# Kernel optimization log

Measured on AMD Instinct MI355X. Metric: run time of the kernel, lower is better.

Reference implementation:

```python
import jax, jax.numpy as jnp
import numpy as np

HEADS = 8
DIM_HEAD = 64
RMS_EPS = 1.1920929e-07  # torch default eps = finfo(fp32).eps


def rotate_half(x):
    x1, x2 = jnp.split(x, 2, axis=-1)
    return jnp.concatenate((-x2, x1), axis=-1)


def setup_inputs() -> dict:
    key = jax.random.key(0)
    k1, k2, k3, k4, k5 = jax.random.split(key, 5)
    b, n, dim = 2, 4096, 1024
    dim_hidden = HEADS * DIM_HEAD  # 512
    x = jax.random.normal(k1, (b, n, dim), dtype=jnp.float32)
    rotary_emb = jax.random.normal(k2, (n, DIM_HEAD), dtype=jnp.float32)
    rms_weight = jnp.ones((dim,), dtype=jnp.float32)
    w_qkv = jax.random.normal(k3, (dim, dim_hidden * 3), dtype=jnp.float32) * (dim ** -0.5)
    w_out = jax.random.normal(k4, (dim_hidden, dim), dtype=jnp.float32) * (dim_hidden ** -0.5)
    return {"x": x, "rotary_emb": rotary_emb, "rms_weight": rms_weight,
            "w_qkv": w_qkv, "w_out": w_out}


def reference(x, rotary_emb, rms_weight, w_qkv, w_out):
    b, n, dim = x.shape
    h, d = HEADS, DIM_HEAD
    # RMSNorm
    xn = x * jax.lax.rsqrt(jnp.mean(x * x, axis=-1, keepdims=True) + RMS_EPS) * rms_weight
    # QKV projection, rearrange 'b n (qkv h d) -> qkv b h n d'
    qkv = (xn @ w_qkv).reshape(b, n, 3, h, d).transpose(2, 0, 3, 1, 4)
    q, k, v = qkv[0], qkv[1], qkv[2]
    # RoPE
    cos, sin = jnp.cos(rotary_emb), jnp.sin(rotary_emb)  # (n, d) broadcasts over b,h
    q = q * cos + rotate_half(q) * sin
    k = k * cos + rotate_half(k) * sin
    q = q * (d ** -0.5)
    sim = jnp.einsum('bhid,bhjd->bhij', q, k)
    causal_mask = jnp.triu(jnp.ones((n, n), dtype=bool), 1)
    sim = jnp.where(causal_mask, -jnp.finfo(sim.dtype).max, sim)
    attn = jax.nn.softmax(sim, axis=-1)
    out = jnp.einsum('bhij,bhjd->bhid', attn, v)
    out = out.transpose(0, 2, 1, 3).reshape(b, n, h * d)  # 'b h n d -> b n (h d)'
    return out @ w_out
```

## Files before the change

kernel.cpp:

```cpp
#include <hip/hip_runtime.h>
#include <hip/hip_bf16.h>
#include <cstdint>

using bf16x8 = __attribute__((ext_vector_type(8))) __bf16;
using f32x4  = __attribute__((ext_vector_type(4))) float;

#define LOG2E 1.4426950408889634f

__device__ inline void gload16(__bf16* lds, const __bf16* g) {
    __builtin_amdgcn_global_load_lds((const __attribute__((address_space(1))) void*)g,
                                     (__attribute__((address_space(3))) void*)lds, 16, 0, 0);
}

__global__ __launch_bounds__(256) void rmsnorm_kernel(const float* __restrict__ x,
                                                      const float* __restrict__ w,
                                                      __bf16* __restrict__ xn) {
    const int row = blockIdx.x;
    const float4 v = reinterpret_cast<const float4*>(x + (size_t)row * 1024)[threadIdx.x];
    float ss = v.x * v.x + v.y * v.y + v.z * v.z + v.w * v.w;
#pragma unroll
    for (int i = 1; i < 64; i <<= 1) ss += __shfl_xor(ss, i);
    __shared__ float part[4];
    if ((threadIdx.x & 63) == 0) part[threadIdx.x >> 6] = ss;
    __syncthreads();
    const float total = part[0] + part[1] + part[2] + part[3];
    const float scale = rsqrtf(total * (1.0f / 1024.0f) + 1.1920929e-07f);
    const float4 wv = reinterpret_cast<const float4*>(w)[threadIdx.x];
    union { __bf16 h[4]; uint2 u; } pk;
    pk.h[0] = (__bf16)(v.x * scale * wv.x);
    pk.h[1] = (__bf16)(v.y * scale * wv.y);
    pk.h[2] = (__bf16)(v.z * scale * wv.z);
    pk.h[3] = (__bf16)(v.w * scale * wv.w);
    reinterpret_cast<uint2*>(xn + (size_t)row * 1024)[threadIdx.x] = pk.u;
}

__global__ void transpose_cast_kernel(const float* __restrict__ in,
                                      __bf16* __restrict__ out, int K, int N) {
    __shared__ float tile[32][33];
    const int n0 = blockIdx.x * 32, k0 = blockIdx.y * 32;
#pragma unroll
    for (int r = threadIdx.y; r < 32; r += 8)
        tile[r][threadIdx.x] = in[(size_t)(k0 + r) * N + n0 + threadIdx.x];
    __syncthreads();
#pragma unroll
    for (int r = threadIdx.y; r < 32; r += 8)
        out[(size_t)(n0 + r) * K + k0 + threadIdx.x] = (__bf16)tile[threadIdx.x][r];
}

__global__ __launch_bounds__(256) void csin_kernel(const float* __restrict__ rot,
                                                   float2* __restrict__ csin) {
    const int i = blockIdx.x * 256 + threadIdx.x;
    float s, c;
    sincosf(rot[i], &s, &c);
    csin[i] = make_float2(c, s);
}

__global__ __launch_bounds__(256) void rope_kernel(__bf16* __restrict__ qk,
                                                   const float2* __restrict__ csin) {
    const int row = blockIdx.x * 4 + (threadIdx.x >> 6);
    const int lane = threadIdx.x & 63;
    const int h = lane >> 3, dl = (lane & 7) * 4;
    const int pos = row & 4095;
    const float4 csA = *reinterpret_cast<const float4*>(&csin[pos * 64 + dl]);
    const float4 csB = *reinterpret_cast<const float4*>(&csin[pos * 64 + dl + 2]);
    const float4 csC = *reinterpret_cast<const float4*>(&csin[pos * 64 + dl + 32]);
    const float4 csD = *reinterpret_cast<const float4*>(&csin[pos * 64 + dl + 34]);
    const float c0[4] = {csA.x, csA.z, csB.x, csB.z};
    const float s0[4] = {csA.y, csA.w, csB.y, csB.w};
    const float c1[4] = {csC.x, csC.z, csD.x, csD.z};
    const float s1[4] = {csC.y, csC.w, csD.y, csD.w};
    __bf16* p = qk + (size_t)row * 1024 + h * 64 + dl;
    const float qs = 0.125f * LOG2E;
#pragma unroll
    for (int part = 0; part < 2; ++part) {
        __bf16* pp = p + part * 512;
        const float sc = part ? 1.0f : qs;
        union { uint2 u; __bf16 hh[4]; } va, vb, oa, ob;
        va.u = *reinterpret_cast<const uint2*>(pp);
        vb.u = *reinterpret_cast<const uint2*>(pp + 32);
#pragma unroll
        for (int j = 0; j < 4; ++j) {
            const float a = (float)va.hh[j], b2 = (float)vb.hh[j];
            oa.hh[j] = (__bf16)((a * c0[j] - b2 * s0[j]) * sc);
            ob.hh[j] = (__bf16)((b2 * c1[j] + a * s1[j]) * sc);
        }
        *reinterpret_cast<uint2*>(pp)      = oa.u;
        *reinterpret_cast<uint2*>(pp + 32) = ob.u;
    }
}

template <typename OutT, int MODE>
__global__ __launch_bounds__(256) void gemm_bt(const __bf16* __restrict__ A,
                                               const __bf16* __restrict__ Bt,
                                               OutT* __restrict__ C,
                                               __bf16* __restrict__ vt,
                                               int M, int N, int K) {
    __shared__ __align__(16) __bf16 As[128 * 32];
    __shared__ __align__(16) __bf16 Bs[128 * 32];
    const int bm = blockIdx.y, bn = blockIdx.x;
    const int tid = threadIdx.x;
    const int w = tid >> 6, l = tid & 63, lg = l >> 4, lr = l & 15;
    const int wr = w >> 1, wc = w & 1;
    const __bf16* Ab = A + (size_t)(bm * 128) * K;
    const __bf16* Bb = Bt + (size_t)(bn * 128) * K;
    const int srow = tid >> 2, scol = (tid & 3) * 8;
    f32x4 acc[4][4] = {};
    for (int k0 = 0; k0 < K; k0 += 32) {
        gload16(As + tid * 8,        Ab + (size_t)srow * K + k0 + scol);
        gload16(As + 2048 + tid * 8, Ab + (size_t)(srow + 64) * K + k0 + scol);
        gload16(Bs + tid * 8,        Bb + (size_t)srow * K + k0 + scol);
        gload16(Bs + 2048 + tid * 8, Bb + (size_t)(srow + 64) * K + k0 + scol);
        __syncthreads();
        bf16x8 af[4], bfr[4];
#pragma unroll
        for (int m = 0; m < 4; ++m)
            af[m] = *reinterpret_cast<const bf16x8*>(&As[(wr * 64 + m * 16 + lr) * 32 + lg * 8]);
#pragma unroll
        for (int nn = 0; nn < 4; ++nn)
            bfr[nn] = *reinterpret_cast<const bf16x8*>(&Bs[(wc * 64 + nn * 16 + lr) * 32 + lg * 8]);
#pragma unroll
        for (int m = 0; m < 4; ++m)
#pragma unroll
            for (int nn = 0; nn < 4; ++nn)
                acc[m][nn] = __builtin_amdgcn_mfma_f32_16x16x32_bf16(af[m], bfr[nn],
                                                                     acc[m][nn], 0, 0, 0);
        __syncthreads();
    }
    if constexpr (MODE == 1) {
        const int cb = bn * 128 + wc * 64;
        if (cb < 1024) {
#pragma unroll
            for (int m = 0; m < 4; ++m) {
                const int rg = bm * 128 + wr * 64 + m * 16 + 4 * lg;
#pragma unroll
                for (int nn = 0; nn < 4; ++nn) {
                    const int cg = cb + nn * 16 + lr;
#pragma unroll
                    for (int r = 0; r < 4; ++r)
                        C[(size_t)(rg + r) * 1024 + cg] = (OutT)acc[m][nn][r];
                }
            }
        } else {
#pragma unroll
            for (int m = 0; m < 4; ++m) {
                const int rg = bm * 128 + wr * 64 + m * 16 + 4 * lg;
                const int bidx = rg >> 12, pos0 = rg & 4095;
                const int a0 = pos0 & 63;
                const int cp = 32 * (a0 >> 5) + 8 * ((a0 >> 2) & 3) + 4 * ((a0 >> 4) & 1);
                const int nbase = (pos0 & ~63) + cp;
#pragma unroll
                for (int nn = 0; nn < 4; ++nn) {
                    const int col = cb + nn * 16 + lr - 1024;
                    const int hh = col >> 6, dd = col & 63;
                    union { __bf16 h4[4]; uint2 u; } pk2;
#pragma unroll
                    for (int r = 0; r < 4; ++r) pk2.h4[r] = (__bf16)acc[m][nn][r];
                    *reinterpret_cast<uint2*>(&vt[((size_t)(bidx * 8 + hh) * 64 + dd) * 4096 + nbase]) = pk2.u;
                }
            }
        }
        return;
    }
#pragma unroll
    for (int m = 0; m < 4; ++m) {
        const int rg = bm * 128 + wr * 64 + m * 16 + 4 * lg;
#pragma unroll
        for (int nn = 0; nn < 4; ++nn) {
            const int cg = bn * 128 + wc * 64 + nn * 16 + lr;
#pragma unroll
            for (int r = 0; r < 4; ++r)
                C[(size_t)(rg + r) * N + cg] = (OutT)acc[m][nn][r];
        }
    }
}

__global__ __launch_bounds__(256) void attn_kernel(const __bf16* __restrict__ qkp,
                                                   const __bf16* __restrict__ vt,
                                                   __bf16* __restrict__ attn_out) {
    const int bid = blockIdx.x;
    const int swz = (bid & 7) * 64 + (bid >> 3);
    const int bh  = swz >> 5;
    const int p   = swz & 31;
    const int b = bh >> 3, h = bh & 7;
    const int tid = threadIdx.x;
    const int w = tid >> 6, l = tid & 63, lg = l >> 4, lr = l & 15;

    __shared__ __align__(16) __bf16 Ks[3][64 * 64];
    __shared__ __align__(16) __bf16 Vs[3][64 * 64];

    const __bf16* qbase = qkp + (size_t)b * 4096 * 1024 + h * 64;
    const __bf16* kbase = qbase + 512;
    const __bf16* vtb   = vt + (size_t)(b * 8 + h) * 64 * 4096;

    const int sr = tid >> 3;
    const int sc = ((tid & 7) ^ (sr & 7)) * 8;
    const __bf16* ksrc0 = kbase + (size_t)sr * 1024 + sc;
    const __bf16* vsrc0 = vtb + (size_t)sr * 4096 + sc;

    const int xel = (lr & 7) * 8;

    for (int seg = 0; seg < 2; ++seg) {
        const int qt = seg ? (63 - p) : p;
        const int wq0 = qt * 64 + 16 * w;
        const int nkt = qt + 1;

        bf16x8 Qf[2];
#pragma unroll
        for (int kh = 0; kh < 2; ++kh)
            Qf[kh] = *reinterpret_cast<const bf16x8*>(
                qbase + (size_t)(wq0 + lr) * 1024 + 32 * kh + 8 * lg);

        f32x4 O[4] = {};
        float m_ = -1e30f, l_ = 0.0f;
        const __bf16* kp = ksrc0;
        const __bf16* vp = vsrc0;

        auto stage2 = [&](__bf16* kdst, __bf16* vdst) {
            gload16(kdst + tid * 8,         kp);
            gload16(kdst + (tid + 256) * 8, kp + 32 * 1024);
            gload16(vdst + tid * 8,         vp);
            gload16(vdst + (tid + 256) * 8, vp + 32 * 4096);
            kp += 64 * 1024;
            vp += 64;
        };
        auto qk_step = [&](f32x4 (&S)[4], const __bf16* kb) {
            __builtin_amdgcn_s_setprio(1);
#pragma unroll
            for (int jt = 0; jt < 4; ++jt) {
                const __bf16* kr = kb + (16 * jt + lr) * 64;
                const bf16x8 Kf0 = *reinterpret_cast<const bf16x8*>(kr + ((8 * lg) ^ xel));
                const bf16x8 Kf1 = *reinterpret_cast<const bf16x8*>(kr + ((32 + 8 * lg) ^ xel));
                f32x4 z = {};
                z = __builtin_amdgcn_mfma_f32_16x16x32_bf16(Kf0, Qf[0], z, 0, 0, 0);
                S[jt] = __builtin_amdgcn_mfma_f32_16x16x32_bf16(Kf1, Qf[1], z, 0, 0, 0);
            }
            __builtin_amdgcn_s_setprio(0);
        };
        auto smpv = [&](f32x4 (&SC)[4], const __bf16* vb, bool domask) {
            if (domask) {
#pragma unroll
                for (int jt = 0; jt < 4; ++jt)
#pragma unroll
                    for (int r = 0; r < 4; ++r)
                        if (16 * jt + 4 * lg + r > 16 * w + lr) SC[jt][r] = -1e30f;
            }
            float mx = -1e30f;
#pragma unroll
            for (int jt = 0; jt < 4; ++jt)
                mx = fmaxf(mx, fmaxf(fmaxf(SC[jt][0], SC[jt][1]), fmaxf(SC[jt][2], SC[jt][3])));
            if (__any(mx > m_ + 8.0f)) {
                mx = fmaxf(mx, __shfl_xor(mx, 16));
                mx = fmaxf(mx, __shfl_xor(mx, 32));
                const float mn = fmaxf(m_, mx);
                const float alpha = __builtin_amdgcn_exp2f(m_ - mn);
                m_ = mn;
                l_ *= alpha;
#pragma unroll
                for (int dt = 0; dt < 4; ++dt) O[dt] *= alpha;
            }
            float sum = 0.0f;
#pragma unroll
            for (int jt = 0; jt < 4; ++jt)
#pragma unroll
                for (int r = 0; r < 4; ++r) {
                    const float pv = __builtin_amdgcn_exp2f(SC[jt][r] - m_);
                    SC[jt][r] = pv;
                    sum += pv;
                }
            l_ += sum;
            __builtin_amdgcn_s_setprio(1);
#pragma unroll
            for (int s = 0; s < 2; ++s) {
                bf16x8 Pf;
#pragma unroll
                for (int i = 0; i < 8; ++i)
                    Pf[i] = (__bf16)SC[2 * s + (i >> 2)][i & 3];
#pragma unroll
                for (int dt = 0; dt < 4; ++dt) {
                    const bf16x8 Vf = *reinterpret_cast<const bf16x8*>(
                        vb + (16 * dt + lr) * 64 + ((32 * s + 8 * lg) ^ xel));
                    O[dt] = __builtin_amdgcn_mfma_f32_16x16x32_bf16(Vf, Pf, O[dt], 0, 0, 0);
                }
            }
            __builtin_amdgcn_s_setprio(0);
        };

        f32x4 S0[4], S1[4];
        int t = 0;

        stage2(Ks[0], Vs[0]);
        stage2(Ks[1], Vs[1]);
        __syncthreads();
        qk_step(S0, Ks[0]);

        for (; t + 8 <= nkt; t += 6) {
            stage2(Ks[2], Vs[2]); qk_step(S1, Ks[1]); smpv(S0, Vs[0], false); __syncthreads();
            stage2(Ks[0], Vs[0]); qk_step(S0, Ks[2]); smpv(S1, Vs[1], false); __syncthreads();
            stage2(Ks[1], Vs[1]); qk_step(S1, Ks[0]); smpv(S0, Vs[2], false); __syncthreads();
            stage2(Ks[2], Vs[2]); qk_step(S0, Ks[1]); smpv(S1, Vs[0], false); __syncthreads();
            stage2(Ks[0], Vs[0]); qk_step(S1, Ks[2]); smpv(S0, Vs[1], false); __syncthreads();
            stage2(Ks[1], Vs[1]); qk_step(S0, Ks[0]); smpv(S1, Vs[2], false); __syncthreads();
        }

        {
            f32x4 Sp[4];
#pragma unroll
            for (int jt = 0; jt < 4; ++jt) Sp[jt] = S0[jt];
            for (; t < nkt; ++t) {
                if (t + 2 < nkt) stage2(Ks[(t + 2) % 3], Vs[(t + 2) % 3]);
                f32x4 Sn[4];
                if (t + 1 < nkt) qk_step(Sn, Ks[(t + 1) % 3]);
                smpv(Sp, Vs[t % 3], t == nkt - 1);
                __syncthreads();
#pragma unroll
                for (int jt = 0; jt < 4; ++jt) Sp[jt] = Sn[jt];
            }
        }

        float lt = l_;
        lt += __shfl_xor(lt, 16);
        lt += __shfl_xor(lt, 32);
        const float inv = 1.0f / lt;
        __bf16* op = attn_out + ((size_t)b * 4096 + wq0 + lr) * 512 + h * 64;
#pragma unroll
        for (int dt = 0; dt < 4; ++dt) {
            union { __bf16 h4[4]; uint2 u; } ow;
#pragma unroll
            for (int r = 0; r < 4; ++r) ow.h4[r] = (__bf16)(O[dt][r] * inv);
            *reinterpret_cast<uint2*>(op + 16 * dt + 4 * lg) = ow.u;
        }
    }
}

extern "C" void kernel_launch(void* const* d_in, const int* in_sizes, int n_in,
                              void* d_out, int out_size, void* d_ws, size_t ws_size,
                              hipStream_t stream) {
    (void)in_sizes; (void)n_in; (void)out_size; (void)ws_size;
    const float* x    = (const float*)d_in[0];
    const float* rot  = (const float*)d_in[1];
    const float* rmsw = (const float*)d_in[2];
    const float* wqkv = (const float*)d_in[3];
    const float* wout = (const float*)d_in[4];
    float* out = (float*)d_out;

    char* ws = (char*)d_ws;
    __bf16* xn    = (__bf16*)ws;
    __bf16* wqkvt = (__bf16*)(ws + 16777216);
    __bf16* woutt = (__bf16*)(ws + 16777216 + 3145728);
    __bf16* aout  = (__bf16*)(ws + 16777216 + 3145728 + 1048576);
    __bf16* qk   = (__bf16*)d_out;
    float2* csin = (float2*)((char*)d_out + 16777216);
    __bf16* vt   = (__bf16*)((char*)d_out + 18874368);

    rmsnorm_kernel<<<8192, 256, 0, stream>>>(x, rmsw, xn);
    transpose_cast_kernel<<<dim3(48, 32), dim3(32, 8), 0, stream>>>(wqkv, wqkvt, 1024, 1536);
    transpose_cast_kernel<<<dim3(32, 16), dim3(32, 8), 0, stream>>>(wout, woutt, 512, 1024);
    csin_kernel<<<1024, 256, 0, stream>>>(rot, csin);
    gemm_bt<__bf16, 1><<<dim3(12, 64), 256, 0, stream>>>(xn, wqkvt, qk, vt, 8192, 1536, 1024);
    rope_kernel<<<2048, 256, 0, stream>>>(qk, csin);
    attn_kernel<<<512, 256, 0, stream>>>(qk, vt, aout);
    gemm_bt<float, 0><<<dim3(8, 64), 256, 0, stream>>>(aout, woutt, out, nullptr, 8192, 1024, 512);
}
```

Before: 147.1 us.

## Deepen async LDS pipelines in GEMM and attention with partial vmcnt waits

The GEMM moves from a single LDS buffer with a load-then-sync each k-step to a 3-stage ring that prefetches two tiles ahead. The attention kernel goes from 3 to 4 K/V buffers and prefetches three tiles ahead. Both replace __syncthreads with an explicit s_waitcnt vmcnt(N) plus s_barrier, so later global-to-LDS loads can stay in flight across the barrier instead of draining every iteration. This hides global load latency behind MFMA work, at the cost of more LDS per block, which may lower occupancy. Correctness also now depends on the hand-chosen vmcnt counts matching the number of outstanding loads.

```diff
diff --git a/kernel.cpp b/kernel.cpp
--- a/kernel.cpp
+++ b/kernel.cpp
@@ -10,6 +10,14 @@
 __device__ inline void gload16(__bf16* lds, const __bf16* g) {
     __builtin_amdgcn_global_load_lds((const __attribute__((address_space(1))) void*)g,
                                      (__attribute__((address_space(3))) void*)lds, 16, 0, 0);
+}
+__device__ inline void wait_barrier4() {
+    asm volatile("s_waitcnt vmcnt(4)" ::: "memory");
+    __builtin_amdgcn_s_barrier();
+}
+__device__ inline void wait_barrier0() {
+    asm volatile("s_waitcnt vmcnt(0)" ::: "memory");
+    __builtin_amdgcn_s_barrier();
 }
 
 __global__ __launch_bounds__(256) void rmsnorm_kernel(const float* __restrict__ x,
@@ -95,8 +103,8 @@
                                                OutT* __restrict__ C,
                                                __bf16* __restrict__ vt,
                                                int M, int N, int K) {
-    __shared__ __align__(16) __bf16 As[128 * 32];
-    __shared__ __align__(16) __bf16 Bs[128 * 32];
+    __shared__ __align__(16) __bf16 As[3][128 * 32];
+    __shared__ __align__(16) __bf16 Bs[3][128 * 32];
     const int bm = blockIdx.y, bn = blockIdx.x;
     const int tid = threadIdx.x;
     const int w = tid >> 6, l = tid & 63, lg = l >> 4, lr = l & 15;
@@ -104,27 +112,43 @@
     const __bf16* Ab = A + (size_t)(bm * 128) * K;
     const __bf16* Bb = Bt + (size_t)(bn * 128) * K;
     const int srow = tid >> 2, scol = (tid & 3) * 8;
+    const __bf16* Asrc = Ab + (size_t)srow * K + scol;
+    const __bf16* Bsrc = Bb + (size_t)srow * K + scol;
+
+    auto stage = [&](int k2) {
+        const int nx = k2 % 3;
+        const int off = k2 * 32;
+        gload16(&As[nx][tid * 8],        Asrc + off);
+        gload16(&As[nx][2048 + tid * 8], Asrc + (size_t)64 * K + off);
+        gload16(&Bs[nx][tid * 8],        Bsrc + off);
+        gload16(&Bs[nx][2048 + tid * 8], Bsrc + (size_t)64 * K + off);
+    };
+
+    const int NS = K >> 5;
     f32x4 acc[4][4] = {};
-    for (int k0 = 0; k0 < K; k0 += 32) {
-        gload16(As + tid * 8,        Ab + (size_t)srow * K + k0 + scol);
-        gload16(As + 2048 + tid * 8, Ab + (size_t)(srow + 64) * K + k0 + scol);
-        gload16(Bs + tid * 8,        Bb + (size_t)srow * K + k0 + scol);
-        gload16(Bs + 2048 + tid * 8, Bb + (size_t)(srow + 64) * K + k0 + scol);
-        __syncthreads();
+    stage(0);
+    stage(1);
+    wait_barrier4();
+    for (int k = 0; k < NS; ++k) {
+        const bool more = (k + 2 < NS);
+        if (more) stage(k + 2);
+        const __bf16* Ac = &As[k % 3][0];
+        const __bf16* Bc = &Bs[k % 3][0];
         bf16x8 af[4], bfr[4];
 #pragma unroll
         for (int m = 0; m < 4; ++m)
-            af[m] = *reinterpret_cast<const bf16x8*>(&As[(wr * 64 + m * 16 + lr) * 32 + lg * 8]);
+            af[m] = *reinterpret_cast<const bf16x8*>(Ac + (wr * 64 + m * 16 + lr) * 32 + lg * 8);
 #pragma unroll
         for (int nn = 0; nn < 4; ++nn)
-            bfr[nn] = *reinterpret_cast<const bf16x8*>(&Bs[(wc * 64 + nn * 16 + lr) * 32 + lg * 8]);
+            bfr[nn] = *reinterpret_cast<const bf16x8*>(Bc + (wc * 64 + nn * 16 + lr) * 32 + lg * 8);
 #pragma unroll
         for (int m = 0; m < 4; ++m)
 #pragma unroll
             for (int nn = 0; nn < 4; ++nn)
                 acc[m][nn] = __builtin_amdgcn_mfma_f32_16x16x32_bf16(af[m], bfr[nn],
                                                                      acc[m][nn], 0, 0, 0);
-        __syncthreads();
+        if (more) wait_barrier4();
+        else      wait_barrier0();
     }
     if constexpr (MODE == 1) {
         const int cb = bn * 128 + wc * 64;
@@ -185,8 +209,8 @@
     const int tid = threadIdx.x;
     const int w = tid >> 6, l = tid & 63, lg = l >> 4, lr = l & 15;
 
-    __shared__ __align__(16) __bf16 Ks[3][64 * 64];
-    __shared__ __align__(16) __bf16 Vs[3][64 * 64];
+    __shared__ __align__(16) __bf16 Ks[4][64 * 64];
+    __shared__ __align__(16) __bf16 Vs[4][64 * 64];
 
     const __bf16* qbase = qkp + (size_t)b * 4096 * 1024 + h * 64;
     const __bf16* kbase = qbase + 512;
@@ -290,16 +314,15 @@
 
         stage2(Ks[0], Vs[0]);
         stage2(Ks[1], Vs[1]);
-        __syncthreads();
+        stage2(Ks[2], Vs[2]);
+        wait_barrier4();
         qk_step(S0, Ks[0]);
 
-        for (; t + 8 <= nkt; t += 6) {
-            stage2(Ks[2], Vs[2]); qk_step(S1, Ks[1]); smpv(S0, Vs[0], false); __syncthreads();
-            stage2(Ks[0], Vs[0]); qk_step(S0, Ks[2]); smpv(S1, Vs[1], false); __syncthreads();
-            stage2(Ks[1], Vs[1]); qk_step(S1, Ks[0]); smpv(S0, Vs[2], false); __syncthreads();
-            stage2(Ks[2], Vs[2]); qk_step(S0, Ks[1]); smpv(S1, Vs[0], false); __syncthreads();
-            stage2(Ks[0], Vs[0]); qk_step(S1, Ks[2]); smpv(S0, Vs[1], false); __syncthreads();
-            stage2(Ks[1], Vs[1]); qk_step(S0, Ks[0]); smpv(S1, Vs[2], false); __syncthreads();
+        for (; t + 8 <= nkt; t += 4) {
+            stage2(Ks[3], Vs[3]); qk_step(S1, Ks[1]); smpv(S0, Vs[0], false); wait_barrier4();
+            stage2(Ks[0], Vs[0]); qk_step(S0, Ks[2]); smpv(S1, Vs[1], false); wait_barrier4();
+            stage2(Ks[1], Vs[1]); qk_step(S1, Ks[3]); smpv(S0, Vs[2], false); wait_barrier4();
+            stage2(Ks[2], Vs[2]); qk_step(S0, Ks[0]); smpv(S1, Vs[3], false); wait_barrier4();
         }
 
         {
@@ -307,11 +330,13 @@
 #pragma unroll
             for (int jt = 0; jt < 4; ++jt) Sp[jt] = S0[jt];
             for (; t < nkt; ++t) {
-                if (t + 2 < nkt) stage2(Ks[(t + 2) % 3], Vs[(t + 2) % 3]);
+                const bool more3 = (t + 3 < nkt);
+                if (more3) stage2(Ks[(t + 3) & 3], Vs[(t + 3) & 3]);
                 f32x4 Sn[4];
-                if (t + 1 < nkt) qk_step(Sn, Ks[(t + 1) % 3]);
-                smpv(Sp, Vs[t % 3], t == nkt - 1);
-                __syncthreads();
+                if (t + 1 < nkt) qk_step(Sn, Ks[(t + 1) & 3]);
+                smpv(Sp, Vs[t & 3], t == nkt - 1);
+                if (more3) wait_barrier4();
+                else       wait_barrier0();
 #pragma unroll
                 for (int jt = 0; jt < 4; ++jt) Sp[jt] = Sn[jt];
             }
```

Result: faster. 142.8 us (-2.9%).
